# Kernel tuning notes

Hardware: AMD Instinct MI355X
Metric: run time of the kernel (lower is better)

The kernel has to match this reference:

```python
import jax, jax.numpy as jnp
import numpy as np

ALPHA = 0.1
BETA = 0.1
N_TASKS = 8
N_ROBOTS = 3
B = 2097152


def setup_inputs() -> dict:
    key = jax.random.key(0)
    k1, k2, k3, k4 = jax.random.split(key, 4)
    predictions = jax.random.normal(k1, (B, N_TASKS * N_ROBOTS), dtype=jnp.float32)
    targets = jax.random.uniform(k2, (B, N_TASKS * N_ROBOTS), dtype=jnp.float32)
    R = jax.random.uniform(k3, (B, N_TASKS, N_ROBOTS), dtype=jnp.float32)  # task capability requirements
    Q = jax.random.uniform(k4, (B, N_ROBOTS, N_ROBOTS), dtype=jnp.float32)  # per-robot capability rows
    return {"predictions": predictions, "targets": targets, "R": R, "Q": Q}


def reference(predictions, targets, R, Q):
    # BCEWithLogitsLoss (mean): softplus(x) - x * t
    base_loss = jnp.mean(jax.nn.softplus(predictions) - predictions * targets)

    b = predictions.shape[0]
    pred_m = predictions.reshape(b, N_TASKS, N_ROBOTS)  # [B, 8, 3]
    # robot assigned to task iff prediction > 0.5 (hard threshold, as in original)
    assigned = (pred_m > 0.5).astype(predictions.dtype)  # [B, 8, 3]
    # total capability per task: sum of Q rows of assigned robots
    total_capability = jnp.einsum('btr,brc->btc', assigned, Q)  # [B, 8, 3]
    shortage = jnp.maximum(R - total_capability, 0.0).sum(-1)  # [B, 8]
    # original only counts tasks where the raw prediction row-sum is > 0
    active = pred_m.sum(-1) > 0.0  # [B, 8]
    capability_violation = jnp.where(active, shortage, 0.0).sum() / b

    time_violation = jnp.asarray(0.0, dtype=predictions.dtype)
    total_loss = base_loss + ALPHA * capability_violation + BETA * time_violation
    return (total_loss, base_loss, capability_violation, time_violation)
```

## Files before the change

### kernel.cpp

```cpp
#include <hip/hip_runtime.h>

#define N_TASKS 8
#define ROW 24
#define ROWB 96
#define TILE 64
#define QROWB 36

typedef __attribute__((address_space(3))) void* lds_ptr_t;
typedef const __attribute__((address_space(1))) void* gbl_ptr_t;

__global__ __launch_bounds__(64) void mrta_partial_kernel(
    const float* __restrict__ pred,
    const float* __restrict__ targ,
    const float* __restrict__ Rm,
    const float* __restrict__ Qm,
    double* __restrict__ partials,
    int B)
{
    __shared__ __align__(16) float4 predL[TILE * 8];
    __shared__ __align__(16) float4 RL[TILE * 8];
    __shared__ __align__(16) float4 QL[192];

    const int l = threadIdx.x;

    int sfix = (l & 7) ^ (l >> 3);
    if (sfix >= 6) sfix = l & 1;
    const int srcPR = ROWB * (l >> 3) + 16 * sfix;

    int pieceIdx[6];
#pragma unroll
    for (int j = 0; j < 6; ++j) {
        int g = j * 64 + l;
        int r = g / 6;
        int s = g - r * 6;
        pieceIdx[j] = 8 * r + (s ^ (r & 7));
    }
    const int key = l & 7;

    double base_acc = 0.0, cap_acc = 0.0;
    const int ntiles = B / TILE;

    for (int tile = blockIdx.x; tile < ntiles; tile += gridDim.x) {
        asm volatile("s_waitcnt lgkmcnt(0)" ::: "memory");
        __builtin_amdgcn_sched_barrier(0);

        const char* predT = (const char*)pred + (size_t)tile * (TILE * ROWB);
        const char* targT = (const char*)targ + (size_t)tile * (TILE * ROWB);
        const char* RT    = (const char*)Rm   + (size_t)tile * (TILE * ROWB);
        const char* QT    = (const char*)Qm   + (size_t)tile * (TILE * QROWB);

        float4 tt[6];
#pragma unroll
        for (int j = 0; j < 6; ++j)
            tt[j] = *(const float4*)(targT + (j * 64 + l) * 16);

#pragma unroll
        for (int j = 0; j < 8; ++j)
            __builtin_amdgcn_global_load_lds((gbl_ptr_t)(predT + j * 768 + srcPR),
                                             (lds_ptr_t)(&predL[j * 64]), 16, 0, 0);
#pragma unroll
        for (int j = 0; j < 8; ++j)
            __builtin_amdgcn_global_load_lds((gbl_ptr_t)(RT + j * 768 + srcPR),
                                             (lds_ptr_t)(&RL[j * 64]), 16, 0, 0);
        __builtin_amdgcn_global_load_lds((gbl_ptr_t)(QT + (0 * 64 + l) * 16),
                                         (lds_ptr_t)(&QL[0]), 16, 0, 0);
        __builtin_amdgcn_global_load_lds((gbl_ptr_t)(QT + (1 * 64 + l) * 16),
                                         (lds_ptr_t)(&QL[64]), 16, 0, 0);
        __builtin_amdgcn_global_load_lds((gbl_ptr_t)(QT + 2048 + (l & 15) * 16),
                                         (lds_ptr_t)(&QL[128]), 16, 0, 0);

        asm volatile("s_waitcnt vmcnt(0)" ::: "memory");
        __builtin_amdgcn_sched_barrier(0);

        float pv[ROW];
#pragma unroll
        for (int s = 0; s < 6; ++s) {
            float4 v = predL[8 * l + (s ^ key)];
            pv[4 * s + 0] = v.x; pv[4 * s + 1] = v.y;
            pv[4 * s + 2] = v.z; pv[4 * s + 3] = v.w;
        }

        float sp0 = 0.0f, sp1 = 0.0f;
#pragma unroll
        for (int i = 0; i < ROW; i += 2) {
            sp0 += fmaxf(pv[i],     0.0f) + __logf(1.0f + __expf(-fabsf(pv[i])));
            sp1 += fmaxf(pv[i + 1], 0.0f) + __logf(1.0f + __expf(-fabsf(pv[i + 1])));
        }

        float rv[ROW];
#pragma unroll
        for (int s = 0; s < 6; ++s) {
            float4 v = RL[8 * l + (s ^ key)];
            rv[4 * s + 0] = v.x; rv[4 * s + 1] = v.y;
            rv[4 * s + 2] = v.z; rv[4 * s + 3] = v.w;
        }

        float qv[9];
        const float* qbase = (const float*)QL;
#pragma unroll
        for (int e = 0; e < 9; ++e) qv[e] = qbase[9 * l + e];

        float cap = 0.0f;
#pragma unroll
        for (int tk = 0; tk < N_TASKS; ++tk) {
            float p0 = pv[tk * 3 + 0];
            float p1 = pv[tk * 3 + 1];
            float p2 = pv[tk * 3 + 2];
            float a0 = (p0 > 0.5f) ? 1.0f : 0.0f;
            float a1 = (p1 > 0.5f) ? 1.0f : 0.0f;
            float a2 = (p2 > 0.5f) ? 1.0f : 0.0f;
            float tc0 = a0 * qv[0] + a1 * qv[3] + a2 * qv[6];
            float tc1 = a0 * qv[1] + a1 * qv[4] + a2 * qv[7];
            float tc2 = a0 * qv[2] + a1 * qv[5] + a2 * qv[8];
            float sh  = fmaxf(rv[tk * 3 + 0] - tc0, 0.0f)
                      + fmaxf(rv[tk * 3 + 1] - tc1, 0.0f)
                      + fmaxf(rv[tk * 3 + 2] - tc2, 0.0f);
            bool active = (p0 + p1 + p2) > 0.0f;
            cap += active ? sh : 0.0f;
        }

        float dt0 = 0.0f, dt1 = 0.0f;
#pragma unroll
        for (int j = 0; j < 6; ++j) {
            float4 pw = predL[pieceIdx[j]];
            dt0 += pw.x * tt[j].x + pw.y * tt[j].y;
            dt1 += pw.z * tt[j].z + pw.w * tt[j].w;
        }

        base_acc += (double)((sp0 + sp1) - (dt0 + dt1));
        cap_acc  += (double)cap;
    }

    if (blockIdx.x == 0) {
        int row = ntiles * TILE + l;
        if (row < B) {
            const float* pr = pred + (size_t)row * ROW;
            const float* tr = targ + (size_t)row * ROW;
            const float* rr = Rm   + (size_t)row * ROW;
            const float* qr = Qm   + (size_t)row * 9;
            float base = 0.0f;
            float pv[ROW];
            for (int i = 0; i < ROW; ++i) {
                float x = pr[i];
                pv[i] = x;
                base += fmaxf(x, 0.0f) + __logf(1.0f + __expf(-fabsf(x))) - x * tr[i];
            }
            float cap = 0.0f;
            for (int tk = 0; tk < N_TASKS; ++tk) {
                float p0 = pv[tk * 3 + 0], p1 = pv[tk * 3 + 1], p2 = pv[tk * 3 + 2];
                float a0 = (p0 > 0.5f) ? 1.0f : 0.0f;
                float a1 = (p1 > 0.5f) ? 1.0f : 0.0f;
                float a2 = (p2 > 0.5f) ? 1.0f : 0.0f;
                float tc0 = a0 * qr[0] + a1 * qr[3] + a2 * qr[6];
                float tc1 = a0 * qr[1] + a1 * qr[4] + a2 * qr[7];
                float tc2 = a0 * qr[2] + a1 * qr[5] + a2 * qr[8];
                float sh  = fmaxf(rr[tk * 3 + 0] - tc0, 0.0f)
                          + fmaxf(rr[tk * 3 + 1] - tc1, 0.0f)
                          + fmaxf(rr[tk * 3 + 2] - tc2, 0.0f);
                if ((p0 + p1 + p2) > 0.0f) cap += sh;
            }
            base_acc += (double)base;
            cap_acc  += (double)cap;
        }
    }

#pragma unroll
    for (int off = 32; off > 0; off >>= 1) {
        base_acc += __shfl_down(base_acc, off);
        cap_acc  += __shfl_down(cap_acc, off);
    }
    if (l == 0) {
        partials[blockIdx.x]             = base_acc;
        partials[gridDim.x + blockIdx.x] = cap_acc;
    }
}

__global__ __launch_bounds__(256) void mrta_final_kernel(
    const double* __restrict__ partials,
    int nparts,
    float* __restrict__ out,
    double inv_BM,
    double inv_B)
{
    double b = 0.0, c = 0.0;
    for (int i = threadIdx.x; i < nparts; i += 256) {
        b += partials[i];
        c += partials[nparts + i];
    }
#pragma unroll
    for (int off = 32; off > 0; off >>= 1) {
        b += __shfl_down(b, off);
        c += __shfl_down(c, off);
    }
    __shared__ double sb[4];
    __shared__ double sc[4];
    const int wave = threadIdx.x >> 6;
    const int lane = threadIdx.x & 63;
    if (lane == 0) { sb[wave] = b; sc[wave] = c; }
    __syncthreads();
    if (threadIdx.x == 0) {
        double bsum = sb[0] + sb[1] + sb[2] + sb[3];
        double csum = sc[0] + sc[1] + sc[2] + sc[3];
        double base = bsum * inv_BM;
        double cap  = csum * inv_B;
        double tot  = base + 0.1 * cap;
        out[0] = (float)tot;
        out[1] = (float)base;
        out[2] = (float)cap;
        out[3] = 0.0f;
    }
}

extern "C" void kernel_launch(void* const* d_in, const int* in_sizes, int n_in,
                              void* d_out, int out_size, void* d_ws, size_t ws_size,
                              hipStream_t stream) {
    const float* pred = (const float*)d_in[0];
    const float* targ = (const float*)d_in[1];
    const float* Rm   = (const float*)d_in[2];
    const float* Qm   = (const float*)d_in[3];
    float* out = (float*)d_out;

    const int B = in_sizes[0] / ROW;

    int blocks = 8192;
    if ((size_t)(2 * blocks) * sizeof(double) > ws_size) {
        blocks = (int)(ws_size / (2 * sizeof(double)));
        if (blocks > 8192) blocks = 8192;
        if (blocks < 1) blocks = 1;
    }

    double* partials = (double*)d_ws;

    mrta_partial_kernel<<<blocks, 64, 0, stream>>>(pred, targ, Rm, Qm, partials, B);
    mrta_final_kernel<<<1, 256, 0, stream>>>(partials, blocks, out,
                                             1.0 / ((double)B * ROW),
                                             1.0 / (double)B);
}
```

Baseline: 133.4 us.

## Double-buffer LDS tile staging to overlap next-tile loads with compute

Restructures the grid-stride loop into a two-stage software pipeline: while one LDS buffer is being consumed, the next tile's pred/R/Q async global-to-LDS loads and target register loads are issued into the other buffer, and a partial vmcnt wait is used before compute. The grid shrinks from 8192 to 2048 blocks so each block handles several tiles and can actually pipeline. This doubles LDS use per block (reducing possible occupancy) and relies on a hand-computed vmcnt count. The Q tail load is also changed to 4-byte per-lane loads.

```diff
diff --git a/kernel.cpp b/kernel.cpp
--- a/kernel.cpp
+++ b/kernel.cpp
@@ -8,6 +8,98 @@
 
 typedef __attribute__((address_space(3))) void* lds_ptr_t;
 typedef const __attribute__((address_space(1))) void* gbl_ptr_t;
+
+#define PRED0 0
+#define R0    512
+#define Q0    1024
+#define BUFSZ 1168
+
+#define SB0 __builtin_amdgcn_sched_barrier(0)
+#define WAITV25 do { asm volatile("s_waitcnt vmcnt(25)" ::: "memory"); } while (0)
+#define WAITV0  do { asm volatile("s_waitcnt vmcnt(0)"  ::: "memory"); } while (0)
+
+#define STAGE(TILEIDX, BSEL) do {                                              \
+    const char* _predT = (const char*)pred + (size_t)(TILEIDX) * (TILE * ROWB);\
+    const char* _RT    = (const char*)Rm   + (size_t)(TILEIDX) * (TILE * ROWB);\
+    const char* _QT    = (const char*)Qm   + (size_t)(TILEIDX) * (TILE * QROWB);\
+    _Pragma("unroll")                                                          \
+    for (int _j = 0; _j < 8; ++_j)                                             \
+        __builtin_amdgcn_global_load_lds((gbl_ptr_t)(_predT + _j * 768 + srcPR),\
+                                         (lds_ptr_t)(&bufL[BSEL][PRED0 + _j * 64]), 16, 0, 0);\
+    _Pragma("unroll")                                                          \
+    for (int _j = 0; _j < 8; ++_j)                                             \
+        __builtin_amdgcn_global_load_lds((gbl_ptr_t)(_RT + _j * 768 + srcPR),  \
+                                         (lds_ptr_t)(&bufL[BSEL][R0 + _j * 64]), 16, 0, 0);\
+    __builtin_amdgcn_global_load_lds((gbl_ptr_t)(_QT + l * 16),                \
+                                     (lds_ptr_t)(&bufL[BSEL][Q0]), 16, 0, 0);  \
+    __builtin_amdgcn_global_load_lds((gbl_ptr_t)(_QT + 1024 + l * 16),         \
+                                     (lds_ptr_t)(&bufL[BSEL][Q0 + 64]), 16, 0, 0);\
+    __builtin_amdgcn_global_load_lds((gbl_ptr_t)(_QT + 2048 + l * 4),          \
+                                     (lds_ptr_t)(&bufL[BSEL][Q0 + 128]), 4, 0, 0);\
+} while (0)
+
+#define LOADT(TT, TILEIDX) do {                                                \
+    const char* _targT = (const char*)targ + (size_t)(TILEIDX) * (TILE * ROWB);\
+    _Pragma("unroll")                                                          \
+    for (int _j = 0; _j < 6; ++_j)                                             \
+        TT[_j] = *(const float4*)(_targT + (_j * 64 + l) * 16);                \
+} while (0)
+
+#define COMPUTE(BSEL, TT) do {                                                 \
+    const float4* _predL = &bufL[BSEL][PRED0];                                 \
+    const float4* _RL    = &bufL[BSEL][R0];                                    \
+    const float* _qbase  = (const float*)&bufL[BSEL][Q0];                      \
+    float pv[ROW];                                                             \
+    _Pragma("unroll")                                                          \
+    for (int _s = 0; _s < 6; ++_s) {                                           \
+        float4 _v = _predL[8 * l + (_s ^ key)];                                \
+        pv[4 * _s + 0] = _v.x; pv[4 * _s + 1] = _v.y;                          \
+        pv[4 * _s + 2] = _v.z; pv[4 * _s + 3] = _v.w;                          \
+    }                                                                          \
+    float _sp0 = 0.0f, _sp1 = 0.0f;                                            \
+    _Pragma("unroll")                                                          \
+    for (int _i = 0; _i < ROW; _i += 2) {                                      \
+        _sp0 += fmaxf(pv[_i],     0.0f) + __logf(1.0f + __expf(-fabsf(pv[_i])));\
+        _sp1 += fmaxf(pv[_i + 1], 0.0f) + __logf(1.0f + __expf(-fabsf(pv[_i + 1])));\
+    }                                                                          \
+    float rv[ROW];                                                             \
+    _Pragma("unroll")                                                          \
+    for (int _s = 0; _s < 6; ++_s) {                                           \
+        float4 _v = _RL[8 * l + (_s ^ key)];                                   \
+        rv[4 * _s + 0] = _v.x; rv[4 * _s + 1] = _v.y;                          \
+        rv[4 * _s + 2] = _v.z; rv[4 * _s + 3] = _v.w;                          \
+    }                                                                          \
+    float qv[9];                                                               \
+    _Pragma("unroll")                                                          \
+    for (int _e = 0; _e < 9; ++_e) qv[_e] = _qbase[9 * l + _e];                \
+    float _cap = 0.0f;                                                         \
+    _Pragma("unroll")                                                          \
+    for (int _tk = 0; _tk < N_TASKS; ++_tk) {                                  \
+        float _p0 = pv[_tk * 3 + 0];                                           \
+        float _p1 = pv[_tk * 3 + 1];                                           \
+        float _p2 = pv[_tk * 3 + 2];                                           \
+        float _a0 = (_p0 > 0.5f) ? 1.0f : 0.0f;                                \
+        float _a1 = (_p1 > 0.5f) ? 1.0f : 0.0f;                                \
+        float _a2 = (_p2 > 0.5f) ? 1.0f : 0.0f;                                \
+        float _tc0 = _a0 * qv[0] + _a1 * qv[3] + _a2 * qv[6];                  \
+        float _tc1 = _a0 * qv[1] + _a1 * qv[4] + _a2 * qv[7];                  \
+        float _tc2 = _a0 * qv[2] + _a1 * qv[5] + _a2 * qv[8];                  \
+        float _sh  = fmaxf(rv[_tk * 3 + 0] - _tc0, 0.0f)                       \
+                   + fmaxf(rv[_tk * 3 + 1] - _tc1, 0.0f)                       \
+                   + fmaxf(rv[_tk * 3 + 2] - _tc2, 0.0f);                      \
+        bool _active = (_p0 + _p1 + _p2) > 0.0f;                               \
+        _cap += _active ? _sh : 0.0f;                                          \
+    }                                                                          \
+    float _dt0 = 0.0f, _dt1 = 0.0f;                                            \
+    _Pragma("unroll")                                                          \
+    for (int _j = 0; _j < 6; ++_j) {                                           \
+        float4 _pw = _predL[pieceIdx[_j]];                                     \
+        _dt0 += _pw.x * TT[_j].x + _pw.y * TT[_j].y;                           \
+        _dt1 += _pw.z * TT[_j].z + _pw.w * TT[_j].w;                           \
+    }                                                                          \
+    base_acc += (double)((_sp0 + _sp1) - (_dt0 + _dt1));                       \
+    cap_acc  += (double)_cap;                                                  \
+} while (0)
 
 __global__ __launch_bounds__(64) void mrta_partial_kernel(
     const float* __restrict__ pred,
@@ -17,9 +109,7 @@
     double* __restrict__ partials,
     int B)
 {
-    __shared__ __align__(16) float4 predL[TILE * 8];
-    __shared__ __align__(16) float4 RL[TILE * 8];
-    __shared__ __align__(16) float4 QL[192];
+    __shared__ __align__(16) float4 bufL[2][BUFSZ];
 
     const int l = threadIdx.x;
 
@@ -38,97 +128,40 @@
     const int key = l & 7;
 
     double base_acc = 0.0, cap_acc = 0.0;
+
+    const int G = gridDim.x;
     const int ntiles = B / TILE;
-
-    for (int tile = blockIdx.x; tile < ntiles; tile += gridDim.x) {
-        asm volatile("s_waitcnt lgkmcnt(0)" ::: "memory");
-        __builtin_amdgcn_sched_barrier(0);
-
-        const char* predT = (const char*)pred + (size_t)tile * (TILE * ROWB);
-        const char* targT = (const char*)targ + (size_t)tile * (TILE * ROWB);
-        const char* RT    = (const char*)Rm   + (size_t)tile * (TILE * ROWB);
-        const char* QT    = (const char*)Qm   + (size_t)tile * (TILE * QROWB);
-
-        float4 tt[6];
-#pragma unroll
-        for (int j = 0; j < 6; ++j)
-            tt[j] = *(const float4*)(targT + (j * 64 + l) * 16);
-
-#pragma unroll
-        for (int j = 0; j < 8; ++j)
-            __builtin_amdgcn_global_load_lds((gbl_ptr_t)(predT + j * 768 + srcPR),
-                                             (lds_ptr_t)(&predL[j * 64]), 16, 0, 0);
-#pragma unroll
-        for (int j = 0; j < 8; ++j)
-            __builtin_amdgcn_global_load_lds((gbl_ptr_t)(RT + j * 768 + srcPR),
-                                             (lds_ptr_t)(&RL[j * 64]), 16, 0, 0);
-        __builtin_amdgcn_global_load_lds((gbl_ptr_t)(QT + (0 * 64 + l) * 16),
-                                         (lds_ptr_t)(&QL[0]), 16, 0, 0);
-        __builtin_amdgcn_global_load_lds((gbl_ptr_t)(QT + (1 * 64 + l) * 16),
-                                         (lds_ptr_t)(&QL[64]), 16, 0, 0);
-        __builtin_amdgcn_global_load_lds((gbl_ptr_t)(QT + 2048 + (l & 15) * 16),
-                                         (lds_ptr_t)(&QL[128]), 16, 0, 0);
-
-        asm volatile("s_waitcnt vmcnt(0)" ::: "memory");
-        __builtin_amdgcn_sched_barrier(0);
-
-        float pv[ROW];
-#pragma unroll
-        for (int s = 0; s < 6; ++s) {
-            float4 v = predL[8 * l + (s ^ key)];
-            pv[4 * s + 0] = v.x; pv[4 * s + 1] = v.y;
-            pv[4 * s + 2] = v.z; pv[4 * s + 3] = v.w;
+    const int t0 = blockIdx.x;
+    const int n = (t0 < ntiles) ? ((ntiles - t0 + G - 1) / G) : 0;
+
+    float4 ttA[6], ttB[6];
+
+    if (n > 0) { STAGE(t0, 0); LOADT(ttA, t0); }
+
+    for (int i = 0; i < n; i += 2) {
+        const int tcur = t0 + i * G;
+        {
+            if (i + 1 < n) {
+                const int tnext = tcur + G;
+                STAGE(tnext, 1); LOADT(ttB, tnext);
+                SB0; WAITV25; SB0;
+            } else {
+                SB0; WAITV0; SB0;
+            }
+            COMPUTE(0, ttA);
+            SB0;
         }
-
-        float sp0 = 0.0f, sp1 = 0.0f;
-#pragma unroll
-        for (int i = 0; i < ROW; i += 2) {
-            sp0 += fmaxf(pv[i],     0.0f) + __logf(1.0f + __expf(-fabsf(pv[i])));
-            sp1 += fmaxf(pv[i + 1], 0.0f) + __logf(1.0f + __expf(-fabsf(pv[i + 1])));
+        if (i + 1 < n) {
+            if (i + 2 < n) {
+                const int tnn = tcur + 2 * G;
+                STAGE(tnn, 0); LOADT(ttA, tnn);
+                SB0; WAITV25; SB0;
+            } else {
+                SB0; WAITV0; SB0;
+            }
+            COMPUTE(1, ttB);
+            SB0;
         }
-
-        float rv[ROW];
-#pragma unroll
-        for (int s = 0; s < 6; ++s) {
-            float4 v = RL[8 * l + (s ^ key)];
-            rv[4 * s + 0] = v.x; rv[4 * s + 1] = v.y;
-            rv[4 * s + 2] = v.z; rv[4 * s + 3] = v.w;
-        }
-
-        float qv[9];
-        const float* qbase = (const float*)QL;
-#pragma unroll
-        for (int e = 0; e < 9; ++e) qv[e] = qbase[9 * l + e];
-
-        float cap = 0.0f;
-#pragma unroll
-        for (int tk = 0; tk < N_TASKS; ++tk) {
-            float p0 = pv[tk * 3 + 0];
-            float p1 = pv[tk * 3 + 1];
-            float p2 = pv[tk * 3 + 2];
-            float a0 = (p0 > 0.5f) ? 1.0f : 0.0f;
-            float a1 = (p1 > 0.5f) ? 1.0f : 0.0f;
-            float a2 = (p2 > 0.5f) ? 1.0f : 0.0f;
-            float tc0 = a0 * qv[0] + a1 * qv[3] + a2 * qv[6];
-            float tc1 = a0 * qv[1] + a1 * qv[4] + a2 * qv[7];
-            float tc2 = a0 * qv[2] + a1 * qv[5] + a2 * qv[8];
-            float sh  = fmaxf(rv[tk * 3 + 0] - tc0, 0.0f)
-                      + fmaxf(rv[tk * 3 + 1] - tc1, 0.0f)
-                      + fmaxf(rv[tk * 3 + 2] - tc2, 0.0f);
-            bool active = (p0 + p1 + p2) > 0.0f;
-            cap += active ? sh : 0.0f;
-        }
-
-        float dt0 = 0.0f, dt1 = 0.0f;
-#pragma unroll
-        for (int j = 0; j < 6; ++j) {
-            float4 pw = predL[pieceIdx[j]];
-            dt0 += pw.x * tt[j].x + pw.y * tt[j].y;
-            dt1 += pw.z * tt[j].z + pw.w * tt[j].w;
-        }
-
-        base_acc += (double)((sp0 + sp1) - (dt0 + dt1));
-        cap_acc  += (double)cap;
     }
 
     if (blockIdx.x == 0) {
@@ -222,10 +255,10 @@
 
     const int B = in_sizes[0] / ROW;
 
-    int blocks = 8192;
+    int blocks = 2048;
     if ((size_t)(2 * blocks) * sizeof(double) > ws_size) {
         blocks = (int)(ws_size / (2 * sizeof(double)));
-        if (blocks > 8192) blocks = 8192;
+        if (blocks > 2048) blocks = 2048;
         if (blocks < 1) blocks = 1;
     }
 
```

Measured after the change: 124.9 us. -6.4%, faster.
